# Optimization experiments

Hardware: AMD Instinct MI355X
Metric: run time of the kernel (lower is better)

The kernel has to match this reference:

```python
import jax, jax.numpy as jnp
import numpy as np

D_MODEL = 512
D_FFN = 2048
N_LAYERS = 6
VOCAB = 1000
D_STATE = 16
D_CONV = 4
D_INNER = 2 * D_MODEL  # expand=2
DT_RANK = 32           # ceil(d_model/16)
B, LT, LS = 2, 512, 512


def _pos_encoding(length, d_model):
    pos = np.arange(length, dtype=np.float32)[:, None]
    div = np.exp(np.arange(0, d_model, 2, dtype=np.float32) * (-np.log(10000.0) / d_model))
    pe = np.zeros((length, d_model), np.float32)
    pe[:, 0::2] = np.sin(pos * div)
    pe[:, 1::2] = np.cos(pos * div)
    return jnp.asarray(pe)


def _layer_norm(x, g, b, eps=1e-6):
    m = x.mean(-1, keepdims=True)
    v = ((x - m) ** 2).mean(-1, keepdims=True)
    return (x - m) * jax.lax.rsqrt(v + eps) * g + b


def _mamba(x, in_w, conv_w, conv_b, xproj_w, dt_w, dt_b, A_log, Dskip, out_w):
    # x: (b, l, d_model)
    b, l, _ = x.shape
    xz = x @ in_w.T                                   # (b, l, 2*d_inner)
    xc, z = jnp.split(xz, 2, axis=-1)
    # causal depthwise conv over time
    xt = jnp.transpose(xc, (0, 2, 1))                 # (b, d_inner, l)
    xt = jnp.pad(xt, ((0, 0), (0, 0), (D_CONV - 1, 0)))
    xt = jax.lax.conv_general_dilated(
        xt, conv_w, window_strides=(1,), padding='VALID',
        feature_group_count=D_INNER, dimension_numbers=('NCH', 'OIH', 'NCH'))
    xc = jax.nn.silu(jnp.transpose(xt, (0, 2, 1)) + conv_b)  # (b, l, d_inner)
    dbl = xc @ xproj_w.T                              # (b, l, dt_rank + 2*n)
    dt, Bm, Cm = jnp.split(dbl, [DT_RANK, DT_RANK + D_STATE], axis=-1)
    dt = jax.nn.softplus(dt @ dt_w.T + dt_b)          # (b, l, d_inner)
    A = -jnp.exp(A_log)                               # (d_inner, n)

    def step(h, xs):
        dt_t, B_t, C_t, u_t = xs                      # (b,d),(b,n),(b,n),(b,d)
        dA = jnp.exp(dt_t[..., None] * A)             # (b, d, n)
        h = dA * h + (dt_t * u_t)[..., None] * B_t[:, None, :]
        y = jnp.einsum('bdn,bn->bd', h, C_t)
        return h, y

    h0 = jnp.zeros((b, D_INNER, D_STATE), x.dtype)
    xs = (jnp.swapaxes(dt, 0, 1), jnp.swapaxes(Bm, 0, 1),
          jnp.swapaxes(Cm, 0, 1), jnp.swapaxes(xc, 0, 1))
    _, ys = jax.lax.scan(step, h0, xs)                # ys: (l, b, d_inner)
    y = jnp.swapaxes(ys, 0, 1) + xc * Dskip
    y = y * jax.nn.silu(z)
    return y @ out_w.T                                # (b, l, d_model)


def setup_inputs() -> dict:
    key = jax.random.key(0)
    ks = iter(jax.random.split(key, 40))

    def rn(shape, s=0.02):
        return jax.random.normal(next(ks), shape, jnp.float32) * s

    def mamba_params():
        return dict(
            in_w=rn((N_LAYERS, 2 * D_INNER, D_MODEL)),
            conv_w=rn((N_LAYERS, D_INNER, 1, D_CONV), 0.1),
            conv_b=rn((N_LAYERS, D_INNER)),
            xproj=rn((N_LAYERS, DT_RANK + 2 * D_STATE, D_INNER)),
            dtw=rn((N_LAYERS, D_INNER, DT_RANK)),
            dtb=rn((N_LAYERS, D_INNER)),
            Alog=jnp.log(jnp.broadcast_to(jnp.arange(1.0, D_STATE + 1.0, dtype=jnp.float32), (N_LAYERS, D_INNER, D_STATE))),
            D=jnp.ones((N_LAYERS, D_INNER), jnp.float32),
            outw=rn((N_LAYERS, D_MODEL, D_INNER)),
        )

    ps, pc = mamba_params(), mamba_params()
    inp = {
        'src': jax.random.normal(next(ks), (B, LS, D_MODEL), jnp.float32),
        'tgt': jax.random.randint(next(ks), (B, LT), 0, VOCAB),
        'emb': rn((VOCAB, D_MODEL)),
        'in_w_s': ps['in_w'], 'conv_w_s': ps['conv_w'], 'conv_b_s': ps['conv_b'],
        'xproj_s': ps['xproj'], 'dtw_s': ps['dtw'], 'dtb_s': ps['dtb'],
        'Alog_s': ps['Alog'], 'D_s': ps['D'], 'outw_s': ps['outw'],
        'in_w_c': pc['in_w'], 'conv_w_c': pc['conv_w'], 'conv_b_c': pc['conv_b'],
        'xproj_c': pc['xproj'], 'dtw_c': pc['dtw'], 'dtb_c': pc['dtb'],
        'Alog_c': pc['Alog'], 'D_c': pc['D'], 'outw_c': pc['outw'],
        'ffn_w1': rn((N_LAYERS, D_FFN, D_MODEL)),
        'ffn_b1': jnp.zeros((N_LAYERS, D_FFN), jnp.float32),
        'ffn_w2': rn((N_LAYERS, D_MODEL, D_FFN)),
        'ffn_b2': jnp.zeros((N_LAYERS, D_MODEL), jnp.float32),
        'ln_g': jnp.ones((N_LAYERS, 3, D_MODEL), jnp.float32),
        'ln_b': jnp.zeros((N_LAYERS, 3, D_MODEL), jnp.float32),
        'fin_g': jnp.ones((D_MODEL,), jnp.float32),
        'fin_b': jnp.zeros((D_MODEL,), jnp.float32),
    }
    return inp


def reference(src, tgt, emb, in_w_s, conv_w_s, conv_b_s, xproj_s, dtw_s, dtb_s,
              Alog_s, D_s, outw_s, in_w_c, conv_w_c, conv_b_c, xproj_c, dtw_c,
              dtb_c, Alog_c, D_c, outw_c, ffn_w1, ffn_b1, ffn_w2, ffn_b2,
              ln_g, ln_b, fin_g, fin_b):
    # NormalizedEmbedding + sinusoidal positional encoding
    x = emb[tgt] * jnp.sqrt(jnp.asarray(D_MODEL, jnp.float32))
    x = x + _pos_encoding(LT, D_MODEL)[None]
    for i in range(N_LAYERS):
        # self mamba (post-norm, normalize_before=False)
        t2 = _mamba(x, in_w_s[i], conv_w_s[i], conv_b_s[i], xproj_s[i],
                    dtw_s[i], dtb_s[i], Alog_s[i], D_s[i], outw_s[i])
        x = _layer_norm(x + t2, ln_g[i, 0], ln_b[i, 0])
        # cross mamba over concat([memory, tgt]) then take last LT steps
        cat = jnp.concatenate([src, x], axis=1)
        t2 = _mamba(cat, in_w_c[i], conv_w_c[i], conv_b_c[i], xproj_c[i],
                    dtw_c[i], dtb_c[i], Alog_c[i], D_c[i], outw_c[i])[:, -LT:]
        x = _layer_norm(x + t2, ln_g[i, 1], ln_b[i, 1])
        # positionwise FFN
        h = jax.nn.relu(x @ ffn_w1[i].T + ffn_b1[i]) @ ffn_w2[i].T + ffn_b2[i]
        x = _layer_norm(x + h, ln_g[i, 2], ln_b[i, 2])
    return _layer_norm(x, fin_g, fin_b)
```

## Files before the change

### kernel.cpp

```cpp
#include <hip/hip_runtime.h>
#include <math.h>

#define DMODEL 512
#define DINNER 1024
#define DSTATE 16
#define DTRANK 32
#define NLAYERS 6
#define BB 2
#define LT 512
#define LS 512

typedef __attribute__((ext_vector_type(8))) short bf16x8;
typedef __attribute__((ext_vector_type(8))) unsigned short u16x8;
typedef __attribute__((ext_vector_type(4))) float f32x4;

__device__ __forceinline__ unsigned short f2bf(float f) {
  unsigned u = __float_as_uint(f);
  u += 0x7fffu + ((u >> 16) & 1u);
  return (unsigned short)(u >> 16);
}
__device__ __forceinline__ float bf2f(unsigned short u) {
  return __uint_as_float((unsigned)u << 16);
}

template<int EPI>
__device__ __forceinline__ float epi_apply(float acc, float b) {
  if (EPI == 1) { float v = acc + b; return v > 0.f ? v : 0.f; }
  if (EPI == 2) { return acc + b; }
  if (EPI == 3) { float v = acc + b; return fmaxf(v, 0.f) + log1pf(__expf(-fabsf(v))); }
  return acc;
}

__global__ __launch_bounds__(256) void cvt_all_kernel(
    const float* __restrict__ i0, const float* __restrict__ i1,
    const float* __restrict__ i2, const float* __restrict__ i3,
    const float* __restrict__ i4, const float* __restrict__ i5,
    const float* __restrict__ i6, const float* __restrict__ i7,
    const float* __restrict__ i8, const float* __restrict__ i9,
    unsigned short* __restrict__ outbase) {
  int i = blockIdx.x * 256 + threadIdx.x;
  if (i >= 8159232) return;
  const float* in; int off;
  if      (i < 1572864) { in = i0; off = i; }
  else if (i < 3145728) { in = i1; off = i - 1572864; }
  else if (i < 3244032) { in = i2; off = i - 3145728; }
  else if (i < 3342336) { in = i3; off = i - 3244032; }
  else if (i < 3391488) { in = i4; off = i - 3342336; }
  else if (i < 3440640) { in = i5; off = i - 3391488; }
  else if (i < 4227072) { in = i6; off = i - 3440640; }
  else if (i < 5013504) { in = i7; off = i - 4227072; }
  else if (i < 6586368) { in = i8; off = i - 5013504; }
  else                  { in = i9; off = i - 6586368; }
  float4 a = ((const float4*)in)[off];
  ushort4 o = make_ushort4(f2bf(a.x), f2bf(a.y), f2bf(a.z), f2bf(a.w));
  *(ushort4*)&outbase[(size_t)i * 4] = o;
}

__global__ __launch_bounds__(256) void embed_cat_kernel(const int* __restrict__ tgt,
    const float* __restrict__ emb, const float* __restrict__ src,
    float* __restrict__ X, unsigned short* __restrict__ Xb,
    unsigned short* __restrict__ CATb) {
  if (blockIdx.x < 2048) {
    int i = blockIdx.x * 256 + threadIdx.x;
    int d = i & (DMODEL - 1);
    int bt = i >> 9;
    int t = bt & (LT - 1);
    int tok = tgt[bt];
    float div = __expf((float)(d & ~1) * (-9.210340371976184f / (float)DMODEL));
    float ang = (float)t * div;
    float pe = (d & 1) ? cosf(ang) : sinf(ang);
    float v = emb[(size_t)tok * DMODEL + d] * 22.627416997969522f + pe;
    X[i] = v;
    Xb[i] = f2bf(v);
  } else {
    int i = (blockIdx.x - 2048) * 256 + threadIdx.x;
    int c8 = (i & 63) * 8;
    int r = i >> 6;
    int b = r >> 9, l = r & 511;
    const float* s = src + ((size_t)b * 512 + l) * DMODEL + c8;
    float4 a = *(const float4*)s;
    float4 bq = *(const float4*)(s + 4);
    u16x8 o;
    o[0] = f2bf(a.x); o[1] = f2bf(a.y); o[2] = f2bf(a.z); o[3] = f2bf(a.w);
    o[4] = f2bf(bq.x); o[5] = f2bf(bq.y); o[6] = f2bf(bq.z); o[7] = f2bf(bq.w);
    *(u16x8*)&CATb[((size_t)b * 1024 + l) * DMODEL + c8] = o;
  }
}

template<int BK, int EPI, bool SPLIT, bool OUTB>
__global__ __launch_bounds__(256) void mgemmA(
    const unsigned short* __restrict__ A, const unsigned short* __restrict__ Bw,
    const float* __restrict__ bias, float* __restrict__ C,
    unsigned short* __restrict__ Cb, int M, int N, int K, int lda) {
  constexpr int PAD = BK + 8;
  constexpr int CHA = BK / 32;
  constexpr int CHB = BK / 16;
  __shared__ __align__(16) unsigned short As[64 * PAD];
  __shared__ __align__(16) unsigned short Bs[128 * PAD];
  const int tid = threadIdx.x;
  const int bn = blockIdx.x * 128;
  const int bm = blockIdx.y * 64;
  const int lane = tid & 63;
  const int w = tid >> 6;
  const int wr = (w >> 1) * 32;
  const int wc = (w & 1) * 64;
  const int l15 = lane & 15;
  const int l4 = lane >> 4;
  const int koff = l4 * 8;
  int kcnt = K, kbeg = 0;
  if (SPLIT) { kcnt = K / (int)gridDim.z; kbeg = blockIdx.z * kcnt; }
  const int nt = kcnt / BK;
  f32x4 acc[2][4] = {};

  int arow_[CHA], ak8_[CHA];
  const unsigned short* Ap[CHA];
#pragma unroll
  for (int i = 0; i < CHA; ++i) {
    int f = tid + 256 * i;
    arow_[i] = f / (BK / 8);
    ak8_[i] = (f % (BK / 8)) * 8;
    Ap[i] = A + (size_t)(bm + arow_[i]) * lda + kbeg + ak8_[i];
  }
  int brow_[CHB], bk8_[CHB];
  const unsigned short* Bp[CHB];
#pragma unroll
  for (int i = 0; i < CHB; ++i) {
    int f = tid + 256 * i;
    brow_[i] = f / (BK / 8);
    bk8_[i] = (f % (BK / 8)) * 8;
    Bp[i] = Bw + (size_t)(bn + brow_[i]) * K + kbeg + bk8_[i];
  }

  u16x8 av[CHA], bv[CHB];
#pragma unroll
  for (int i = 0; i < CHA; ++i) av[i] = *(const u16x8*)Ap[i];
#pragma unroll
  for (int i = 0; i < CHB; ++i) bv[i] = *(const u16x8*)Bp[i];

  for (int t = 0; t < nt; ++t) {
    __syncthreads();
#pragma unroll
    for (int i = 0; i < CHA; ++i) *(u16x8*)&As[arow_[i] * PAD + ak8_[i]] = av[i];
#pragma unroll
    for (int i = 0; i < CHB; ++i) *(u16x8*)&Bs[brow_[i] * PAD + bk8_[i]] = bv[i];
    if (t + 1 < nt) {
      int ko = (t + 1) * BK;
#pragma unroll
      for (int i = 0; i < CHA; ++i) av[i] = *(const u16x8*)(Ap[i] + ko);
#pragma unroll
      for (int i = 0; i < CHB; ++i) bv[i] = *(const u16x8*)(Bp[i] + ko);
    }
    __syncthreads();
#pragma unroll
    for (int kk = 0; kk < BK / 32; ++kk) {
      bf16x8 afr[2], bfr[4];
#pragma unroll
      for (int i = 0; i < 2; ++i)
        afr[i] = *(const bf16x8*)&As[(wr + i * 16 + l15) * PAD + kk * 32 + koff];
#pragma unroll
      for (int j = 0; j < 4; ++j)
        bfr[j] = *(const bf16x8*)&Bs[(wc + j * 16 + l15) * PAD + kk * 32 + koff];
#pragma unroll
      for (int fr = 0; fr < 2; ++fr)
#pragma unroll
        for (int fc = 0; fc < 4; ++fc)
          acc[fr][fc] = __builtin_amdgcn_mfma_f32_16x16x32_bf16(
              afr[fr], bfr[fc], acc[fr][fc], 0, 0, 0);
    }
  }

  if (SPLIT) {
    unsigned short* Pz = Cb + (size_t)blockIdx.z * M * N;
#pragma unroll
    for (int fc = 0; fc < 4; ++fc) {
      int col = bn + wc + fc * 16 + l15;
#pragma unroll
      for (int fr = 0; fr < 2; ++fr) {
        int row0 = bm + wr + fr * 16 + l4 * 4;
#pragma unroll
        for (int r = 0; r < 4; ++r)
          Pz[(size_t)(row0 + r) * N + col] = f2bf(acc[fr][fc][r]);
      }
    }
  } else {
#pragma unroll
    for (int fc = 0; fc < 4; ++fc) {
      int col = bn + wc + fc * 16 + l15;
      float bvs = (EPI != 0) ? bias[col] : 0.f;
#pragma unroll
      for (int fr = 0; fr < 2; ++fr) {
        int row0 = bm + wr + fr * 16 + l4 * 4;
#pragma unroll
        for (int r = 0; r < 4; ++r) {
          float v = epi_apply<EPI>(acc[fr][fc][r], bvs);
          if (OUTB) Cb[(size_t)(row0 + r) * N + col] = f2bf(v);
          else      C[(size_t)(row0 + r) * N + col] = v;
        }
      }
    }
  }
}

template<int BK, int EPI, bool SPLIT, bool OUTB>
__global__ __launch_bounds__(256) void mgemm(
    const unsigned short* __restrict__ A, const unsigned short* __restrict__ Bw,
    const float* __restrict__ bias, float* __restrict__ C,
    unsigned short* __restrict__ Cb, int M, int N, int K, int lda) {
  constexpr int PAD = BK + 8;
  constexpr int CH = BK / 32;
  __shared__ __align__(16) unsigned short As[64 * PAD];
  __shared__ __align__(16) unsigned short Bs[64 * PAD];
  const int tid = threadIdx.x;
  const int bn = blockIdx.x * 64;
  const int bm = blockIdx.y * 64;
  const int lane = tid & 63;
  const int w = tid >> 6;
  const int wr = (w >> 1) * 32;
  const int wc = (w & 1) * 32;
  const int l15 = lane & 15;
  const int l4 = lane >> 4;
  const int koff = l4 * 8;
  int kcnt = K, kbeg = 0;
  if (SPLIT) { kcnt = K / (int)gridDim.z; kbeg = blockIdx.z * kcnt; }
  const int nt = kcnt / BK;
  f32x4 acc[2][2] = {};

  int row_[CH], k8_[CH];
  const unsigned short *Ap[CH], *Bp[CH];
#pragma unroll
  for (int i = 0; i < CH; ++i) {
    int f = tid + 256 * i;
    row_[i] = f / (BK / 8);
    k8_[i] = (f % (BK / 8)) * 8;
    Ap[i] = A + (size_t)(bm + row_[i]) * lda + kbeg + k8_[i];
    Bp[i] = Bw + (size_t)(bn + row_[i]) * K + kbeg + k8_[i];
  }

  u16x8 av[CH], bv[CH];
#pragma unroll
  for (int i = 0; i < CH; ++i) { av[i] = *(const u16x8*)Ap[i]; bv[i] = *(const u16x8*)Bp[i]; }

  for (int t = 0; t < nt; ++t) {
    __syncthreads();
#pragma unroll
    for (int i = 0; i < CH; ++i) {
      *(u16x8*)&As[row_[i] * PAD + k8_[i]] = av[i];
      *(u16x8*)&Bs[row_[i] * PAD + k8_[i]] = bv[i];
    }
    if (t + 1 < nt) {
      int ko = (t + 1) * BK;
#pragma unroll
      for (int i = 0; i < CH; ++i) {
        av[i] = *(const u16x8*)(Ap[i] + ko);
        bv[i] = *(const u16x8*)(Bp[i] + ko);
      }
    }
    __syncthreads();
#pragma unroll
    for (int kk = 0; kk < CH; ++kk) {
      bf16x8 afr[2], bfr[2];
#pragma unroll
      for (int i = 0; i < 2; ++i) {
        afr[i] = *(const bf16x8*)&As[(wr + i * 16 + l15) * PAD + kk * 32 + koff];
        bfr[i] = *(const bf16x8*)&Bs[(wc + i * 16 + l15) * PAD + kk * 32 + koff];
      }
#pragma unroll
      for (int fr = 0; fr < 2; ++fr)
#pragma unroll
        for (int fc = 0; fc < 2; ++fc)
          acc[fr][fc] = __builtin_amdgcn_mfma_f32_16x16x32_bf16(
              afr[fr], bfr[fc], acc[fr][fc], 0, 0, 0);
    }
  }

  if (SPLIT) {
    float* Pz = C + (size_t)blockIdx.z * M * N;
#pragma unroll
    for (int fc = 0; fc < 2; ++fc) {
      int col = bn + wc + fc * 16 + l15;
#pragma unroll
      for (int fr = 0; fr < 2; ++fr) {
        int row0 = bm + wr + fr * 16 + l4 * 4;
#pragma unroll
        for (int r = 0; r < 4; ++r)
          Pz[(size_t)(row0 + r) * N + col] = acc[fr][fc][r];
      }
    }
  } else {
#pragma unroll
    for (int fc = 0; fc < 2; ++fc) {
      int col = bn + wc + fc * 16 + l15;
      float bvs = (EPI != 0) ? bias[col] : 0.f;
#pragma unroll
      for (int fr = 0; fr < 2; ++fr) {
        int row0 = bm + wr + fr * 16 + l4 * 4;
#pragma unroll
        for (int r = 0; r < 4; ++r) {
          float v = epi_apply<EPI>(acc[fr][fc][r], bvs);
          if (OUTB) Cb[(size_t)(row0 + r) * N + col] = f2bf(v);
          else      C[(size_t)(row0 + r) * N + col] = v;
        }
      }
    }
  }
}

__global__ __launch_bounds__(256) void conv_silu_kernel(
    const unsigned short* __restrict__ xzb, const float* __restrict__ w,
    const float* __restrict__ bias, unsigned short* __restrict__ outb, int L) {
  int idx = blockIdx.x * 256 + threadIdx.x;
  int d8 = (idx & 127) * 8;
  int bt = idx >> 7;
  int b = bt / L;
  int t = bt - b * L;
  const unsigned short* col = xzb + ((size_t)b * L) * (2 * DINNER) + d8;
  float acc[8];
  float4 wv[8];
#pragma unroll
  for (int j = 0; j < 8; ++j) {
    acc[j] = bias[d8 + j];
    wv[j] = *(const float4*)(w + (size_t)(d8 + j) * 4);
  }
#pragma unroll
  for (int k = 0; k < 4; ++k) {
    int tt = t - 3 + k;
    if (tt >= 0) {
      u16x8 v = *(const u16x8*)(col + (size_t)tt * (2 * DINNER));
      float wk[8] = {
        k == 0 ? wv[0].x : k == 1 ? wv[0].y : k == 2 ? wv[0].z : wv[0].w,
        k == 0 ? wv[1].x : k == 1 ? wv[1].y : k == 2 ? wv[1].z : wv[1].w,
        k == 0 ? wv[2].x : k == 1 ? wv[2].y : k == 2 ? wv[2].z : wv[2].w,
        k == 0 ? wv[3].x : k == 1 ? wv[3].y : k == 2 ? wv[3].z : wv[3].w,
        k == 0 ? wv[4].x : k == 1 ? wv[4].y : k == 2 ? wv[4].z : wv[4].w,
        k == 0 ? wv[5].x : k == 1 ? wv[5].y : k == 2 ? wv[5].z : wv[5].w,
        k == 0 ? wv[6].x : k == 1 ? wv[6].y : k == 2 ? wv[6].z : wv[6].w,
        k == 0 ? wv[7].x : k == 1 ? wv[7].y : k == 2 ? wv[7].z : wv[7].w };
#pragma unroll
      for (int j = 0; j < 8; ++j) acc[j] = fmaf(bf2f(v[j]), wk[j], acc[j]);
    }
  }
  u16x8 o;
#pragma unroll
  for (int j = 0; j < 8; ++j) {
    float sig = 1.f / (1.f + __expf(-acc[j]));
    o[j] = f2bf(acc[j] * sig);
  }
  *(u16x8*)&outb[(size_t)bt * DINNER + d8] = o;
}

__global__ __launch_bounds__(256) void scan_pass1(
    const float* __restrict__ XPP, const unsigned short* __restrict__ u,
    const float* __restrict__ Alog, const float* __restrict__ dtw,
    const float* __restrict__ dtb, float* __restrict__ P, float* __restrict__ S,
    int L, int CL) {
  __shared__ float DBL8[32][64];
  const int tid = threadIdx.x;
  const int d = blockIdx.x * 256 + tid;
  const int b = blockIdx.y;
  const int c = blockIdx.z;
  const int t0 = c * CL;
  if (tid < CL * 8) {
    int t = tid >> 3, j8 = (tid & 7) * 8;
    const float* p = XPP + ((size_t)b * L + t0 + t) * 64 + j8;
    const size_t zs = (size_t)BB * L * 64;
    float s[8] = {0.f, 0.f, 0.f, 0.f, 0.f, 0.f, 0.f, 0.f};
#pragma unroll
    for (int z = 0; z < 8; ++z) {
      float4 a = *(const float4*)(p + z * zs);
      float4 bq = *(const float4*)(p + z * zs + 4);
      s[0] += a.x; s[1] += a.y; s[2] += a.z; s[3] += a.w;
      s[4] += bq.x; s[5] += bq.y; s[6] += bq.z; s[7] += bq.w;
    }
#pragma unroll
    for (int j = 0; j < 8; ++j) DBL8[t][j8 + j] = s[j];
  }
  float A[16];
#pragma unroll
  for (int j = 0; j < 4; ++j) {
    float4 a4 = *(const float4*)(Alog + d * 16 + j * 4);
    A[j * 4 + 0] = -__expf(a4.x); A[j * 4 + 1] = -__expf(a4.y);
    A[j * 4 + 2] = -__expf(a4.z); A[j * 4 + 3] = -__expf(a4.w);
  }
  float wreg[32];
#pragma unroll
  for (int j = 0; j < 8; ++j) {
    float4 w4 = *(const float4*)(dtw + (size_t)d * 32 + j * 4);
    wreg[j*4+0] = w4.x; wreg[j*4+1] = w4.y; wreg[j*4+2] = w4.z; wreg[j*4+3] = w4.w;
  }
  float dtbv = dtb[d];
  float h[16], Pp[16];
#pragma unroll
  for (int n = 0; n < 16; ++n) { h[n] = 0.f; Pp[n] = 1.f; }
  const unsigned short* up = u + ((size_t)b * L + t0) * DINNER + d;
  __syncthreads();
  for (int t = 0; t < CL; ++t) {
    float dtraw = dtbv;
#pragma unroll
    for (int k8 = 0; k8 < 8; ++k8) {
      float4 q = *(const float4*)&DBL8[t][k8 * 4];
      dtraw = fmaf(q.x, wreg[k8*4+0], dtraw);
      dtraw = fmaf(q.y, wreg[k8*4+1], dtraw);
      dtraw = fmaf(q.z, wreg[k8*4+2], dtraw);
      dtraw = fmaf(q.w, wreg[k8*4+3], dtraw);
    }
    float dtv = fmaxf(dtraw, 0.f) + log1pf(__expf(-fabsf(dtraw)));
    float uv = bf2f(up[(size_t)t * DINNER]);
    float du = dtv * uv;
    float Bv[16];
#pragma unroll
    for (int j = 0; j < 4; ++j) {
      float4 b4 = *(const float4*)&DBL8[t][32 + j * 4];
      Bv[j*4+0] = b4.x; Bv[j*4+1] = b4.y; Bv[j*4+2] = b4.z; Bv[j*4+3] = b4.w;
    }
#pragma unroll
    for (int n = 0; n < 16; ++n) {
      float dA = __expf(dtv * A[n]);
      Pp[n] *= dA;
      h[n] = fmaf(dA, h[n], du * Bv[n]);
    }
  }
  size_t base = (size_t)c * 32768 + ((size_t)(b * 1024 + d) << 4);
#pragma unroll
  for (int j = 0; j < 4; ++j) {
    *(float4*)&P[base + j * 4] = make_float4(Pp[j*4], Pp[j*4+1], Pp[j*4+2], Pp[j*4+3]);
    *(float4*)&S[base + j * 4] = make_float4(h[j*4], h[j*4+1], h[j*4+2], h[j*4+3]);
  }
}

__global__ __launch_bounds__(256) void scan_pass2(
    const float* __restrict__ XPP, const unsigned short* __restrict__ u,
    const unsigned short* __restrict__ xzb, const float* __restrict__ Alog,
    const float* __restrict__ dtw, const float* __restrict__ dtb,
    const float* __restrict__ Dsk, const float* __restrict__ P,
    const float* __restrict__ S, unsigned short* __restrict__ ysb,
    int L, int CL, int c0) {
  __shared__ float DBL8[32][64];
  const int tid = threadIdx.x;
  const int d = blockIdx.x * 256 + tid;
  const int b = blockIdx.y;
  const int c = blockIdx.z + c0;
  const int t0 = c * CL;
  if (tid < CL * 8) {
    int t = tid >> 3, j8 = (tid & 7) * 8;
    const float* p = XPP + ((size_t)b * L + t0 + t) * 64 + j8;
    const size_t zs = (size_t)BB * L * 64;
    float s[8] = {0.f, 0.f, 0.f, 0.f, 0.f, 0.f, 0.f, 0.f};
#pragma unroll
    for (int z = 0; z < 8; ++z) {
      float4 a = *(const float4*)(p + z * zs);
      float4 bq = *(const float4*)(p + z * zs + 4);
      s[0] += a.x; s[1] += a.y; s[2] += a.z; s[3] += a.w;
      s[4] += bq.x; s[5] += bq.y; s[6] += bq.z; s[7] += bq.w;
    }
#pragma unroll
    for (int j = 0; j < 8; ++j) DBL8[t][j8 + j] = s[j];
  }
  float A[16];
#pragma unroll
  for (int j = 0; j < 4; ++j) {
    float4 a4 = *(const float4*)(Alog + d * 16 + j * 4);
    A[j * 4 + 0] = -__expf(a4.x); A[j * 4 + 1] = -__expf(a4.y);
    A[j * 4 + 2] = -__expf(a4.z); A[j * 4 + 3] = -__expf(a4.w);
  }
  float wreg[32];
#pragma unroll
  for (int j = 0; j < 8; ++j) {
    float4 w4 = *(const float4*)(dtw + (size_t)d * 32 + j * 4);
    wreg[j*4+0] = w4.x; wreg[j*4+1] = w4.y; wreg[j*4+2] = w4.z; wreg[j*4+3] = w4.w;
  }
  float dtbv = dtb[d];
  float h[16];
#pragma unroll
  for (int n = 0; n < 16; ++n) h[n] = 0.f;
  size_t sbase = (size_t)(b * 1024 + d) << 4;
  for (int cc = 0; cc < c; ++cc) {
    size_t bb = (size_t)cc * 32768 + sbase;
#pragma unroll
    for (int j = 0; j < 4; ++j) {
      float4 p4 = *(const float4*)&P[bb + j * 4];
      float4 s4 = *(const float4*)&S[bb + j * 4];
      h[j*4+0] = fmaf(p4.x, h[j*4+0], s4.x);
      h[j*4+1] = fmaf(p4.y, h[j*4+1], s4.y);
      h[j*4+2] = fmaf(p4.z, h[j*4+2], s4.z);
      h[j*4+3] = fmaf(p4.w, h[j*4+3], s4.w);
    }
  }
  float Dv = Dsk[d];
  const unsigned short* up = u + ((size_t)b * L + t0) * DINNER + d;
  const unsigned short* zp = xzb + ((size_t)b * L + t0) * (2 * DINNER) + DINNER + d;
  unsigned short* yp = ysb + ((size_t)(b * 512) + (t0 - c0 * CL)) * DINNER + d;
  __syncthreads();
  for (int t = 0; t < CL; ++t) {
    float dtraw = dtbv;
#pragma unroll
    for (int k8 = 0; k8 < 8; ++k8) {
      float4 q = *(const float4*)&DBL8[t][k8 * 4];
      dtraw = fmaf(q.x, wreg[k8*4+0], dtraw);
      dtraw = fmaf(q.y, wreg[k8*4+1], dtraw);
      dtraw = fmaf(q.z, wreg[k8*4+2], dtraw);
      dtraw = fmaf(q.w, wreg[k8*4+3], dtraw);
    }
    float dtv = fmaxf(dtraw, 0.f) + log1pf(__expf(-fabsf(dtraw)));
    float uv = bf2f(up[(size_t)t * DINNER]);
    float zv = bf2f(zp[(size_t)t * (2 * DINNER)]);
    float du = dtv * uv;
    float Bv[16], Cv[16];
#pragma unroll
    for (int j = 0; j < 4; ++j) {
      float4 b4 = *(const float4*)&DBL8[t][32 + j * 4];
      float4 c4 = *(const float4*)&DBL8[t][48 + j * 4];
      Bv[j*4+0] = b4.x; Bv[j*4+1] = b4.y; Bv[j*4+2] = b4.z; Bv[j*4+3] = b4.w;
      Cv[j*4+0] = c4.x; Cv[j*4+1] = c4.y; Cv[j*4+2] = c4.z; Cv[j*4+3] = c4.w;
    }
    float y = 0.f;
#pragma unroll
    for (int n = 0; n < 16; ++n) {
      float dA = __expf(dtv * A[n]);
      h[n] = fmaf(dA, h[n], du * Bv[n]);
      y = fmaf(h[n], Cv[n], y);
    }
    float sig = 1.f / (1.f + __expf(-zv));
    yp[(size_t)t * DINNER] = f2bf((y + uv * Dv) * (zv * sig));
  }
}

template<int NZ, int EPI, bool FIN>
__global__ __launch_bounds__(64) void ln_red_kernel(
    const float* __restrict__ res, const unsigned short* __restrict__ Pb,
    const float* __restrict__ bias, const float* __restrict__ g,
    const float* __restrict__ be, float* __restrict__ out,
    unsigned short* __restrict__ outb, int row_scale, int row_off,
    const float* __restrict__ fing, const float* __restrict__ finb,
    float* __restrict__ fout) {
  int r = blockIdx.x;
  int b = r >> 9, t = r & 511;
  int lane = threadIdx.x;
  const float* rp = res + (size_t)r * DMODEL;
  size_t ob = ((size_t)(b * row_scale + row_off + t)) * DMODEL;
  float v[8];
  float s = 0.f, ss = 0.f;
#pragma unroll
  for (int j = 0; j < 8; ++j) {
    int col = lane + j * 64;
    float acc = 0.f;
#pragma unroll
    for (int z = 0; z < NZ; ++z)
      acc += bf2f(Pb[(size_t)z * 524288 + (size_t)r * DMODEL + col]);
    float bv = (EPI != 0) ? bias[col] : 0.f;
    float x = rp[col] + epi_apply<EPI>(acc, bv);
    v[j] = x; s += x; ss += x * x;
  }
#pragma unroll
  for (int o = 32; o > 0; o >>= 1) { s += __shfl_xor(s, o); ss += __shfl_xor(ss, o); }
  float m = s * (1.f / 512.f);
  float var = ss * (1.f / 512.f) - m * m;
  float rs = rsqrtf(var + 1e-6f);
  if (FIN) {
    float o2[8];
    float s2 = 0.f, ss2 = 0.f;
#pragma unroll
    for (int j = 0; j < 8; ++j) {
      int col = lane + j * 64;
      float x = (v[j] - m) * rs * g[col] + be[col];
      o2[j] = x; s2 += x; ss2 += x * x;
    }
#pragma unroll
    for (int o = 32; o > 0; o >>= 1) { s2 += __shfl_xor(s2, o); ss2 += __shfl_xor(ss2, o); }
    float m2 = s2 * (1.f / 512.f);
    float var2 = ss2 * (1.f / 512.f) - m2 * m2;
    float rs2 = rsqrtf(var2 + 1e-6f);
#pragma unroll
    for (int j = 0; j < 8; ++j) {
      int col = lane + j * 64;
      fout[(size_t)r * DMODEL + col] = (o2[j] - m2) * rs2 * fing[col] + finb[col];
    }
  } else {
#pragma unroll
    for (int j = 0; j < 8; ++j) {
      int col = lane + j * 64;
      float o2 = (v[j] - m) * rs * g[col] + be[col];
      out[(size_t)r * DMODEL + col] = o2;
      outb[ob + col] = f2bf(o2);
    }
  }
}

extern "C" void kernel_launch(void* const* d_in, const int* in_sizes, int n_in,
                              void* d_out, int out_size, void* d_ws, size_t ws_size,
                              hipStream_t stream) {
  (void)in_sizes; (void)n_in; (void)out_size; (void)ws_size;
  const float* src      = (const float*)d_in[0];
  const int*   tgt      = (const int*)d_in[1];
  const float* emb      = (const float*)d_in[2];
  const float* in_w_s   = (const float*)d_in[3];
  const float* conv_w_s = (const float*)d_in[4];
  const float* conv_b_s = (const float*)d_in[5];
  const float* xproj_s  = (const float*)d_in[6];
  const float* dtw_s    = (const float*)d_in[7];
  const float* dtb_s    = (const float*)d_in[8];
  const float* Alog_s   = (const float*)d_in[9];
  const float* D_s      = (const float*)d_in[10];
  const float* outw_s   = (const float*)d_in[11];
  const float* in_w_c   = (const float*)d_in[12];
  const float* conv_w_c = (const float*)d_in[13];
  const float* conv_b_c = (const float*)d_in[14];
  const float* xproj_c  = (const float*)d_in[15];
  const float* dtw_c    = (const float*)d_in[16];
  const float* dtb_c    = (const float*)d_in[17];
  const float* Alog_c   = (const float*)d_in[18];
  const float* D_c      = (const float*)d_in[19];
  const float* outw_c   = (const float*)d_in[20];
  const float* ffn_w1   = (const float*)d_in[21];
  const float* ffn_b1   = (const float*)d_in[22];
  const float* ffn_w2   = (const float*)d_in[23];
  const float* ffn_b2   = (const float*)d_in[24];
  const float* ln_g     = (const float*)d_in[25];
  const float* ln_b     = (const float*)d_in[26];
  const float* fin_g    = (const float*)d_in[27];
  const float* fin_b    = (const float*)d_in[28];

  float* ws   = (float*)d_ws;
  float* X    = ws;
  float* XPP  = X + 524288;
  float* SC_P = XPP + 1048576;
  float* SC_S = SC_P + 1048576;
  unsigned short* U = (unsigned short*)(SC_S + 1048576);
  unsigned short* Xb   = U;
  unsigned short* CATb = Xb + 524288;
  unsigned short* XCb  = CATb + 1048576;
  unsigned short* XZb  = XCb + 2097152;
  unsigned short* YSb  = XZb + 4194304;
  unsigned short* XZPb = YSb + 1048576;
  unsigned short* WB   = XZPb + 4194304;
  unsigned short* inwsb = WB;
  unsigned short* inwcb = inwsb + 6291456;
  unsigned short* xpsb  = inwcb + 6291456;
  unsigned short* xpcb  = xpsb + 393216;
  unsigned short* dtwsb = xpcb + 393216;
  unsigned short* dtwcb = dtwsb + 196608;
  unsigned short* owsb  = dtwcb + 196608;
  unsigned short* owcb  = owsb + 3145728;
  unsigned short* f1b   = owcb + 3145728;
  unsigned short* f2b   = f1b + 6291456;

  cvt_all_kernel<<<31872, 256, 0, stream>>>(
      in_w_s, in_w_c, xproj_s, xproj_c, dtw_s, dtw_c, outw_s, outw_c,
      ffn_w1, ffn_w2, WB);
  embed_cat_kernel<<<2304, 256, 0, stream>>>(tgt, emb, src, X, Xb, CATb);

  for (int i = 0; i < NLAYERS; ++i) {
    mgemm<64, 0, false, true><<<dim3(32, 16), 256, 0, stream>>>(
        Xb, inwsb + (size_t)i * 1048576, nullptr, nullptr, XZb, 1024, 2048, 512, 512);
    conv_silu_kernel<<<512, 256, 0, stream>>>(
        XZb, conv_w_s + (size_t)i * 4096, conv_b_s + (size_t)i * 1024, XCb, 512);
    mgemm<64, 0, true, false><<<dim3(1, 16, 8), 256, 0, stream>>>(
        XCb, xpsb + (size_t)i * 65536, nullptr, XPP, nullptr, 1024, 64, 1024, 1024);
    scan_pass1<<<dim3(4, 2, 32), 256, 0, stream>>>(
        XPP, XCb, Alog_s + (size_t)i * 16384, dtw_s + (size_t)i * 32768,
        dtb_s + (size_t)i * 1024, SC_P, SC_S, 512, 16);
    scan_pass2<<<dim3(4, 2, 32), 256, 0, stream>>>(
        XPP, XCb, XZb, Alog_s + (size_t)i * 16384, dtw_s + (size_t)i * 32768,
        dtb_s + (size_t)i * 1024, D_s + (size_t)i * 1024, SC_P, SC_S, YSb, 512, 16, 0);
    mgemmA<64, 0, true, false><<<dim3(4, 16, 8), 256, 0, stream>>>(
        YSb, owsb + (size_t)i * 524288, nullptr, nullptr, XZPb, 1024, 512, 1024, 1024);
    ln_red_kernel<8, 0, false><<<1024, 64, 0, stream>>>(
        X, XZPb, nullptr, ln_g + (size_t)(i * 3 + 0) * 512,
        ln_b + (size_t)(i * 3 + 0) * 512, X, CATb, 1024, 512,
        nullptr, nullptr, nullptr);

    mgemmA<64, 0, false, true><<<dim3(16, 32), 256, 0, stream>>>(
        CATb, inwcb + (size_t)i * 1048576, nullptr, nullptr, XZb, 2048, 2048, 512, 512);
    conv_silu_kernel<<<1024, 256, 0, stream>>>(
        XZb, conv_w_c + (size_t)i * 4096, conv_b_c + (size_t)i * 1024, XCb, 1024);
    mgemm<64, 0, true, false><<<dim3(1, 32, 8), 256, 0, stream>>>(
        XCb, xpcb + (size_t)i * 65536, nullptr, XPP, nullptr, 2048, 64, 1024, 1024);
    scan_pass1<<<dim3(4, 2, 32), 256, 0, stream>>>(
        XPP, XCb, Alog_c + (size_t)i * 16384, dtw_c + (size_t)i * 32768,
        dtb_c + (size_t)i * 1024, SC_P, SC_S, 1024, 32);
    scan_pass2<<<dim3(4, 2, 16), 256, 0, stream>>>(
        XPP, XCb, XZb, Alog_c + (size_t)i * 16384, dtw_c + (size_t)i * 32768,
        dtb_c + (size_t)i * 1024, D_c + (size_t)i * 1024, SC_P, SC_S, YSb, 1024, 32, 16);
    mgemmA<64, 0, true, false><<<dim3(4, 16, 8), 256, 0, stream>>>(
        YSb, owcb + (size_t)i * 524288, nullptr, nullptr, XZPb, 1024, 512, 1024, 1024);
    ln_red_kernel<8, 0, false><<<1024, 64, 0, stream>>>(
        X, XZPb, nullptr, ln_g + (size_t)(i * 3 + 1) * 512,
        ln_b + (size_t)(i * 3 + 1) * 512, X, Xb, 512, 0,
        nullptr, nullptr, nullptr);

    mgemm<64, 1, false, true><<<dim3(32, 16), 256, 0, stream>>>(
        Xb, f1b + (size_t)i * 1048576, ffn_b1 + (size_t)i * 2048, nullptr, XZb,
        1024, 2048, 512, 512);
    mgemmA<64, 0, true, false><<<dim3(4, 16, 8), 256, 0, stream>>>(
        XZb, f2b + (size_t)i * 1048576, nullptr, nullptr, XZPb, 1024, 512, 2048, 2048);
    if (i < NLAYERS - 1) {
      ln_red_kernel<8, 2, false><<<1024, 64, 0, stream>>>(
          X, XZPb, ffn_b2 + (size_t)i * 512, ln_g + (size_t)(i * 3 + 2) * 512,
          ln_b + (size_t)(i * 3 + 2) * 512, X, Xb, 512, 0,
          nullptr, nullptr, nullptr);
    } else {
      ln_red_kernel<8, 2, true><<<1024, 64, 0, stream>>>(
          X, XZPb, ffn_b2 + (size_t)i * 512, ln_g + (size_t)(i * 3 + 2) * 512,
          ln_b + (size_t)(i * 3 + 2) * 512, nullptr, nullptr, 512, 0,
          fin_g, fin_b, (float*)d_out);
    }
  }
}
```

Measured before the change: 1.130 ms.

## Load GEMM tiles directly into LDS with global_load_lds and XOR swizzle

Both bf16 MFMA GEMM kernels now copy their A and B tiles from global memory straight into LDS using the global_load_lds builtin, instead of staging them through registers. The padded LDS layout is replaced by an unpadded one whose 16-byte chunks are XOR-swizzled by row, to avoid bank conflicts on the fragment reads. The aim is to cut register pressure and the instructions spent on staging copies. In exchange, the old register prefetch of the next tile is dropped, so loads no longer overlap with MFMA work. The per-wave address mapping also assumes a particular BK tile size.

New measurement: 1.157 ms. +2.4%, slower.

```diff
diff --git a/kernel.cpp b/kernel.cpp
--- a/kernel.cpp
+++ b/kernel.cpp
@@ -21,6 +21,12 @@
 }
 __device__ __forceinline__ float bf2f(unsigned short u) {
   return __uint_as_float((unsigned)u << 16);
+}
+
+__device__ __forceinline__ void gl16(const unsigned short* g, unsigned short* l) {
+  __builtin_amdgcn_global_load_lds(
+      (const __attribute__((address_space(1))) void*)g,
+      (__attribute__((address_space(3))) void*)l, 16, 0, 0);
 }
 
 template<int EPI>
@@ -92,74 +98,68 @@
     const unsigned short* __restrict__ A, const unsigned short* __restrict__ Bw,
     const float* __restrict__ bias, float* __restrict__ C,
     unsigned short* __restrict__ Cb, int M, int N, int K, int lda) {
-  constexpr int PAD = BK + 8;
-  constexpr int CHA = BK / 32;
-  constexpr int CHB = BK / 16;
-  __shared__ __align__(16) unsigned short As[64 * PAD];
-  __shared__ __align__(16) unsigned short Bs[128 * PAD];
+  constexpr int RSB = BK * 2;
+  constexpr int SM = RSB / 16 - 1;
+  __shared__ __align__(16) unsigned short As[64 * BK];
+  __shared__ __align__(16) unsigned short Bs[128 * BK];
   const int tid = threadIdx.x;
   const int bn = blockIdx.x * 128;
   const int bm = blockIdx.y * 64;
   const int lane = tid & 63;
-  const int w = tid >> 6;
-  const int wr = (w >> 1) * 32;
-  const int wc = (w & 1) * 64;
+  const int wv = tid >> 6;
+  const int wr = ((tid >> 6) >> 1) * 32;
+  const int wc = ((tid >> 6) & 1) * 64;
   const int l15 = lane & 15;
   const int l4 = lane >> 4;
-  const int koff = l4 * 8;
   int kcnt = K, kbeg = 0;
   if (SPLIT) { kcnt = K / (int)gridDim.z; kbeg = blockIdx.z * kcnt; }
   const int nt = kcnt / BK;
   f32x4 acc[2][4] = {};
 
-  int arow_[CHA], ak8_[CHA];
-  const unsigned short* Ap[CHA];
-#pragma unroll
-  for (int i = 0; i < CHA; ++i) {
-    int f = tid + 256 * i;
-    arow_[i] = f / (BK / 8);
-    ak8_[i] = (f % (BK / 8)) * 8;
-    Ap[i] = A + (size_t)(bm + arow_[i]) * lda + kbeg + ak8_[i];
-  }
-  int brow_[CHB], bk8_[CHB];
-  const unsigned short* Bp[CHB];
-#pragma unroll
-  for (int i = 0; i < CHB; ++i) {
-    int f = tid + 256 * i;
-    brow_[i] = f / (BK / 8);
-    bk8_[i] = (f % (BK / 8)) * 8;
-    Bp[i] = Bw + (size_t)(bn + brow_[i]) * K + kbeg + bk8_[i];
-  }
-
-  u16x8 av[CHA], bv[CHB];
-#pragma unroll
-  for (int i = 0; i < CHA; ++i) av[i] = *(const u16x8*)Ap[i];
-#pragma unroll
-  for (int i = 0; i < CHB; ++i) bv[i] = *(const u16x8*)Bp[i];
+  const unsigned short* AG[2];
+  unsigned short* AL[2];
+#pragma unroll
+  for (int q = 0; q < 2; ++q) {
+    int s = wv * 2048 + q * 1024 + lane * 16;
+    int row = s / RSB;
+    int cb = (s % RSB) ^ ((row & SM) << 4);
+    AG[q] = A + (size_t)(bm + row) * lda + kbeg + (cb >> 1);
+    AL[q] = &As[(wv * 2048 + q * 1024) >> 1];
+  }
+  const unsigned short* BG[4];
+  unsigned short* BL[4];
+#pragma unroll
+  for (int q = 0; q < 4; ++q) {
+    int s = wv * 4096 + q * 1024 + lane * 16;
+    int row = s / RSB;
+    int cb = (s % RSB) ^ ((row & SM) << 4);
+    BG[q] = Bw + (size_t)(bn + row) * K + kbeg + (cb >> 1);
+    BL[q] = &Bs[(wv * 4096 + q * 1024) >> 1];
+  }
 
   for (int t = 0; t < nt; ++t) {
     __syncthreads();
-#pragma unroll
-    for (int i = 0; i < CHA; ++i) *(u16x8*)&As[arow_[i] * PAD + ak8_[i]] = av[i];
-#pragma unroll
-    for (int i = 0; i < CHB; ++i) *(u16x8*)&Bs[brow_[i] * PAD + bk8_[i]] = bv[i];
-    if (t + 1 < nt) {
-      int ko = (t + 1) * BK;
-#pragma unroll
-      for (int i = 0; i < CHA; ++i) av[i] = *(const u16x8*)(Ap[i] + ko);
-#pragma unroll
-      for (int i = 0; i < CHB; ++i) bv[i] = *(const u16x8*)(Bp[i] + ko);
-    }
+    int ko = t * BK;
+#pragma unroll
+    for (int q = 0; q < 2; ++q) gl16(AG[q] + ko, AL[q]);
+#pragma unroll
+    for (int q = 0; q < 4; ++q) gl16(BG[q] + ko, BL[q]);
     __syncthreads();
 #pragma unroll
     for (int kk = 0; kk < BK / 32; ++kk) {
       bf16x8 afr[2], bfr[4];
 #pragma unroll
-      for (int i = 0; i < 2; ++i)
-        afr[i] = *(const bf16x8*)&As[(wr + i * 16 + l15) * PAD + kk * 32 + koff];
-#pragma unroll
-      for (int j = 0; j < 4; ++j)
-        bfr[j] = *(const bf16x8*)&Bs[(wc + j * 16 + l15) * PAD + kk * 32 + koff];
+      for (int i = 0; i < 2; ++i) {
+        int row = wr + i * 16 + l15;
+        int bo = row * RSB + ((kk * 64 + l4 * 16) ^ ((row & SM) << 4));
+        afr[i] = *(const bf16x8*)((const char*)As + bo);
+      }
+#pragma unroll
+      for (int j = 0; j < 4; ++j) {
+        int row = wc + j * 16 + l15;
+        int bo = row * RSB + ((kk * 64 + l4 * 16) ^ ((row & SM) << 4));
+        bfr[j] = *(const bf16x8*)((const char*)Bs + bo);
+      }
 #pragma unroll
       for (int fr = 0; fr < 2; ++fr)
 #pragma unroll
@@ -206,63 +206,54 @@
     const unsigned short* __restrict__ A, const unsigned short* __restrict__ Bw,
     const float* __restrict__ bias, float* __restrict__ C,
     unsigned short* __restrict__ Cb, int M, int N, int K, int lda) {
-  constexpr int PAD = BK + 8;
-  constexpr int CH = BK / 32;
-  __shared__ __align__(16) unsigned short As[64 * PAD];
-  __shared__ __align__(16) unsigned short Bs[64 * PAD];
+  constexpr int RSB = BK * 2;
+  constexpr int SM = RSB / 16 - 1;
+  __shared__ __align__(16) unsigned short As[64 * BK];
+  __shared__ __align__(16) unsigned short Bs[64 * BK];
   const int tid = threadIdx.x;
   const int bn = blockIdx.x * 64;
   const int bm = blockIdx.y * 64;
   const int lane = tid & 63;
-  const int w = tid >> 6;
-  const int wr = (w >> 1) * 32;
-  const int wc = (w & 1) * 32;
+  const int wv = tid >> 6;
+  const int wr = (wv >> 1) * 32;
+  const int wc = (wv & 1) * 32;
   const int l15 = lane & 15;
   const int l4 = lane >> 4;
-  const int koff = l4 * 8;
   int kcnt = K, kbeg = 0;
   if (SPLIT) { kcnt = K / (int)gridDim.z; kbeg = blockIdx.z * kcnt; }
   const int nt = kcnt / BK;
   f32x4 acc[2][2] = {};
 
-  int row_[CH], k8_[CH];
-  const unsigned short *Ap[CH], *Bp[CH];
-#pragma unroll
-  for (int i = 0; i < CH; ++i) {
-    int f = tid + 256 * i;
-    row_[i] = f / (BK / 8);
-    k8_[i] = (f % (BK / 8)) * 8;
-    Ap[i] = A + (size_t)(bm + row_[i]) * lda + kbeg + k8_[i];
-    Bp[i] = Bw + (size_t)(bn + row_[i]) * K + kbeg + k8_[i];
-  }
-
-  u16x8 av[CH], bv[CH];
-#pragma unroll
-  for (int i = 0; i < CH; ++i) { av[i] = *(const u16x8*)Ap[i]; bv[i] = *(const u16x8*)Bp[i]; }
+  const unsigned short *AG[2], *BG[2];
+  unsigned short *AL[2], *BL[2];
+#pragma unroll
+  for (int q = 0; q < 2; ++q) {
+    int s = wv * 2048 + q * 1024 + lane * 16;
+    int row = s / RSB;
+    int cb = (s % RSB) ^ ((row & SM) << 4);
+    AG[q] = A + (size_t)(bm + row) * lda + kbeg + (cb >> 1);
+    BG[q] = Bw + (size_t)(bn + row) * K + kbeg + (cb >> 1);
+    AL[q] = &As[(wv * 2048 + q * 1024) >> 1];
+    BL[q] = &Bs[(wv * 2048 + q * 1024) >> 1];
+  }
 
   for (int t = 0; t < nt; ++t) {
     __syncthreads();
-#pragma unroll
-    for (int i = 0; i < CH; ++i) {
-      *(u16x8*)&As[row_[i] * PAD + k8_[i]] = av[i];
-      *(u16x8*)&Bs[row_[i] * PAD + k8_[i]] = bv[i];
-    }
-    if (t + 1 < nt) {
-      int ko = (t + 1) * BK;
-#pragma unroll
-      for (int i = 0; i < CH; ++i) {
-        av[i] = *(const u16x8*)(Ap[i] + ko);
-        bv[i] = *(const u16x8*)(Bp[i] + ko);
-      }
-    }
+    int ko = t * BK;
+#pragma unroll
+    for (int q = 0; q < 2; ++q) { gl16(AG[q] + ko, AL[q]); gl16(BG[q] + ko, BL[q]); }
     __syncthreads();
 #pragma unroll
-    for (int kk = 0; kk < CH; ++kk) {
+    for (int kk = 0; kk < BK / 32; ++kk) {
       bf16x8 afr[2], bfr[2];
 #pragma unroll
       for (int i = 0; i < 2; ++i) {
-        afr[i] = *(const bf16x8*)&As[(wr + i * 16 + l15) * PAD + kk * 32 + koff];
-        bfr[i] = *(const bf16x8*)&Bs[(wc + i * 16 + l15) * PAD + kk * 32 + koff];
+        int rowA = wr + i * 16 + l15;
+        int boA = rowA * RSB + ((kk * 64 + l4 * 16) ^ ((rowA & SM) << 4));
+        afr[i] = *(const bf16x8*)((const char*)As + boA);
+        int rowB = wc + i * 16 + l15;
+        int boB = rowB * RSB + ((kk * 64 + l4 * 16) ^ ((rowB & SM) << 4));
+        bfr[i] = *(const bf16x8*)((const char*)Bs + boB);
       }
 #pragma unroll
       for (int fr = 0; fr < 2; ++fr)
```
